# Performance work log

Measured on AMD Instinct MI355X. Metric: run time of the kernel, lower is better.

Reference implementation:

```python
import jax, jax.numpy as jnp
import numpy as np

H = 3072; NH = 24; HD = 128; MLP_D = 12288
B = 1; IMG = 1536; REF = 512; TXT = 256

def _gelu_tanh(x):
    return jax.nn.gelu(x, approximate=True)

def _ln(x, eps=1e-6):
    m = jnp.mean(x, axis=-1, keepdims=True)
    v = jnp.var(x, axis=-1, keepdims=True)
    return (x - m) * jax.lax.rsqrt(v + eps)

def _rms(x, g, eps=1e-6):
    return x * jax.lax.rsqrt(jnp.mean(x * x, axis=-1, keepdims=True) + eps) * g

def _rot_half(x):
    # interleaved rotate-half: (x0,x1,x2,x3,...) -> (-x1,x0,-x3,x2,...)
    x2 = x.reshape(x.shape[:-1] + (-1, 2))
    return jnp.stack([-x2[..., 1], x2[..., 0]], axis=-1).reshape(x.shape)

def setup_inputs():
    key = jax.random.key(0)
    ks = jax.random.split(key, 16)
    s = 0.02
    # rope tables for image tokens (interleaved layout, values repeated x2)
    inv_freq = 1.0 / (10000.0 ** (jnp.arange(0, HD // 2, dtype=jnp.float32) / (HD // 2)))
    ang = jnp.arange(IMG, dtype=jnp.float32)[:, None] * inv_freq[None, :]   # [IMG, HD//2]
    ang = jnp.repeat(ang, 2, axis=-1)                                       # [IMG, HD]
    return {
        'x':   jax.random.normal(ks[0], (B, IMG + TXT, H), jnp.float32),
        'vec': jax.random.normal(ks[1], (B, H), jnp.float32),
        'ref': jax.random.normal(ks[2], (B, REF, H), jnp.float32),
        'cos': jnp.cos(ang), 'sin': jnp.sin(ang),
        'mod_w':  jax.random.normal(ks[3], (H, 3 * H), jnp.float32) * s,
        'mod_b':  jnp.zeros((3 * H,), jnp.float32),
        'rf1_w':  jax.random.normal(ks[4], (H, H), jnp.float32) * s,
        'rf1_b':  jnp.zeros((H,), jnp.float32),
        'rf2_w':  jax.random.normal(ks[5], (H, H), jnp.float32) * s,
        'rf2_b':  jnp.zeros((H,), jnp.float32),
        'rln_g':  jnp.ones((H,), jnp.float32),
        'rln_b':  jnp.zeros((H,), jnp.float32),
        'lin1_w': jax.random.normal(ks[6], (H, 3 * H + MLP_D), jnp.float32) * s,
        'lin1_b': jnp.zeros((3 * H + MLP_D,), jnp.float32),
        'q_g':    jnp.ones((HD,), jnp.float32),
        'k_g':    jnp.ones((HD,), jnp.float32),
        'lin2_w': jax.random.normal(ks[7], (H + MLP_D, H), jnp.float32) * s,
        'lin2_b': jnp.zeros((H,), jnp.float32),
        'text_mask': jnp.ones((B, TXT), jnp.int32),
        'img_len': IMG, 'txt_len': TXT,
    }

def _forward(x, vec, ref, cos, sin, mod_w, mod_b, rf1_w, rf1_b, rf2_w, rf2_b,
             rln_g, rln_b, lin1_w, lin1_b, q_g, k_g, lin2_w, lin2_b,
             text_mask, img_len, txt_len):
    Bb = x.shape[0]
    ref_len = ref.shape[1]
    # modulation (ModulateDiT: SiLU -> Linear -> chunk(3))
    mod = jnp.dot(jax.nn.silu(vec), mod_w) + mod_b
    shift, scale, gate = jnp.split(mod, 3, axis=-1)
    x_mod = _ln(x) * (1.0 + scale[:, None]) + shift[:, None]
    # ref MLP + affine LayerNorm
    r = jnp.dot(_gelu_tanh(jnp.dot(ref, rf1_w) + rf1_b), rf2_w) + rf2_b
    r = _ln(r) * rln_g + rln_b
    # token reassembly: [img | ref | txt]
    xc = jnp.concatenate([x_mod[:, :img_len], r, x_mod[:, img_len:]], axis=1)
    h = jnp.dot(xc, lin1_w) + lin1_b
    qkv, mlp = h[..., :3 * H], h[..., 3 * H:]
    L2 = xc.shape[1]
    q, k, v = [t.reshape(Bb, L2, NH, HD) for t in jnp.split(qkv, 3, axis=-1)]
    # q drops the ref span; ref contributes K/V only
    q = jnp.concatenate([q[:, :img_len], q[:, img_len + ref_len:]], axis=1)
    q = _rms(q, q_g)
    k = _rms(k, k_g)
    # rotary only on image tokens
    c = cos[None, :, None, :]; s = sin[None, :, None, :]
    img_q = q[:, :img_len] * c + _rot_half(q[:, :img_len]) * s
    img_k = k[:, :img_len] * c + _rot_half(k[:, :img_len]) * s
    q = jnp.concatenate([img_q, q[:, img_len:]], axis=1)          # [B, Lq, NH, HD]
    k = jnp.concatenate([img_k, k[:, img_len:]], axis=1)          # [B, Lkv, NH, HD]
    # varlen mask (cu_seqlens semantics): valid attends valid, pad attends pad
    tmask = text_mask.astype(bool)
    qv  = jnp.concatenate([jnp.ones((Bb, img_len), bool), tmask], axis=1)
    kvv = jnp.concatenate([jnp.ones((Bb, img_len + ref_len), bool), tmask], axis=1)
    allowed = (qv[:, None, :, None] == kvv[:, None, None, :])     # [B,1,Lq,Lkv]
    scores = jnp.einsum('bqhd,bkhd->bhqk', q, k) * (HD ** -0.5)
    scores = jnp.where(allowed, scores, jnp.asarray(-1e9, scores.dtype))
    p = jax.nn.softmax(scores, axis=-1)
    attn = jnp.einsum('bhqk,bkhd->bqhd', p, v).reshape(Bb, img_len + txt_len, H)
    mlp = jnp.concatenate([mlp[:, :img_len], mlp[:, img_len + ref_len:]], axis=1)
    out = jnp.dot(jnp.concatenate([attn, _gelu_tanh(mlp)], axis=-1), lin2_w) + lin2_b
    return x + out * gate[:, None]

def reference(x, vec, ref, cos, sin, mod_w, mod_b, rf1_w, rf1_b, rf2_w, rf2_b,
              rln_g, rln_b, lin1_w, lin1_b, q_g, k_g, lin2_w, lin2_b,
              text_mask, img_len, txt_len):
    return _forward(x, vec, ref, cos, sin, mod_w, mod_b, rf1_w, rf1_b, rf2_w, rf2_b,
                    rln_g, rln_b, lin1_w, lin1_b, q_g, k_g, lin2_w, lin2_b,
                    text_mask, img_len, txt_len)
```

## Files before the change

kernel.cpp:

```cpp
#include <hip/hip_runtime.h>
#include <cstdint>
#include <cstddef>

typedef unsigned short u16;
typedef unsigned int   u32;
typedef __bf16 bf16_t;
typedef bf16_t bf16x8 __attribute__((ext_vector_type(8)));
typedef float  f32x4  __attribute__((ext_vector_type(4)));
typedef u16    u16x4  __attribute__((ext_vector_type(4)));


__device__ __forceinline__ float b2f(u16 b){ u32 u=((u32)b)<<16; float f; __builtin_memcpy(&f,&u,4); return f; }
__device__ __forceinline__ u16 f2b(float f){ u32 u; __builtin_memcpy(&u,&f,4); u = u + 0x7fffu + ((u>>16)&1u); return (u16)(u>>16); }
__device__ __forceinline__ float gelu_f(float x){
  float x3 = x*x*x;
  return 0.5f*x*(1.f + tanhf(0.7978845608028654f*(x + 0.044715f*x3)));
}

__device__ __forceinline__ void gload_lds16(const void* g, void* l){
  __builtin_amdgcn_global_load_lds((const __attribute__((address_space(1))) void*)g,
                                   (__attribute__((address_space(3))) void*)l, 16, 0, 0);
}

template<int NW, bool MX>
__device__ __forceinline__ float bred(float v, float* red){
  #pragma unroll
  for (int o=32;o;o>>=1){ float u=__shfl_down(v,o,64); v = MX? fmaxf(v,u) : v+u; }
  const int t = threadIdx.x;
  if ((t&63)==0) red[t>>6]=v;
  __syncthreads();
  float r = red[0];
  #pragma unroll
  for (int i=1;i<NW;i++) r = MX? fmaxf(r,red[i]) : r+red[i];
  __syncthreads();
  return r;
}

__device__ __forceinline__ void unpack8(uint4 u, float* f){
  f[0]=b2f((u16)(u.x&0xffffu)); f[1]=b2f((u16)(u.x>>16));
  f[2]=b2f((u16)(u.y&0xffffu)); f[3]=b2f((u16)(u.y>>16));
  f[4]=b2f((u16)(u.z&0xffffu)); f[5]=b2f((u16)(u.z>>16));
  f[6]=b2f((u16)(u.w&0xffffu)); f[7]=b2f((u16)(u.w>>16));
}
__device__ __forceinline__ uint4 pack8(const float* f){
  uint4 u;
  u.x = (u32)f2b(f[0]) | ((u32)f2b(f[1])<<16);
  u.y = (u32)f2b(f[2]) | ((u32)f2b(f[3])<<16);
  u.z = (u32)f2b(f[4]) | ((u32)f2b(f[5])<<16);
  u.w = (u32)f2b(f[6]) | ((u32)f2b(f[7])<<16);
  return u;
}

__global__ void modv_part(const float* __restrict__ vec, const float* __restrict__ W,
                          float* __restrict__ part){
  __shared__ float s[128];
  const int t = threadIdx.x;
  const int j = blockIdx.x*256 + t;
  const int i0 = blockIdx.y*128;
  if (t < 128){ float v = vec[i0+t]; s[t] = v/(1.f+__expf(-v)); }
  __syncthreads();
  float acc = 0.f;
  #pragma unroll 8
  for (int i=0;i<128;i++) acc += s[i]*W[(size_t)(i0+i)*9216 + j];
  part[(size_t)blockIdx.y*9216 + j] = acc;
}
__global__ void modv_reduce(const float* __restrict__ part, const float* __restrict__ mb,
                            float* __restrict__ modp){
  const int j = blockIdx.x*256 + threadIdx.x;
  float a = mb[j];
  #pragma unroll
  for (int c=0;c<24;c++) a += part[(size_t)c*9216 + j];
  modp[j] = a;
}

__global__ void convT(const float* __restrict__ W, u16* __restrict__ Wt, int Kd, int Nd){
  __shared__ float Ls[32][33];
  const int tx = threadIdx.x, ty = threadIdx.y;
  const int n0 = blockIdx.x*32, k0 = blockIdx.y*32;
  #pragma unroll
  for (int r=0;r<4;r++) Ls[ty+r*8][tx] = W[(size_t)(k0+ty+r*8)*Nd + n0+tx];
  __syncthreads();
  #pragma unroll
  for (int r=0;r<4;r++) Wt[(size_t)(n0+ty+r*8)*Kd + k0+tx] = f2b(Ls[tx][ty+r*8]);
}

__global__ void convertF2B(const float* __restrict__ src, u16* __restrict__ dst){
  const size_t i = ((size_t)blockIdx.x*256 + threadIdx.x)*4;
  const float4 v = *(const float4*)(src+i);
  u16x4 o; o.x=f2b(v.x); o.y=f2b(v.y); o.z=f2b(v.z); o.w=f2b(v.w);
  *(u16x4*)(dst+i) = o;
}

__global__ void ln_modulate(const float* __restrict__ x, const float* __restrict__ modp,
                            u16* __restrict__ xc){
  __shared__ float red[4];
  const int row = blockIdx.x, t = threadIdx.x;
  const float* xr = x + (size_t)row*3072;
  float4 v[3]; float s=0.f, ss=0.f;
  #pragma unroll
  for (int k=0;k<3;k++){
    v[k] = *(const float4*)(xr + t*4 + k*1024);
    s  += v[k].x+v[k].y+v[k].z+v[k].w;
    ss += v[k].x*v[k].x+v[k].y*v[k].y+v[k].z*v[k].z+v[k].w*v[k].w;
  }
  s  = bred<4,false>(s, red);
  ss = bred<4,false>(ss, red);
  const float mean = s*(1.f/3072.f);
  const float inv = rsqrtf(ss*(1.f/3072.f)-mean*mean + 1e-6f);
  const int orow = row<1536 ? row : row+512;
  u16* o = xc + (size_t)orow*3072;
  const float* shiftp = modp; const float* scalep = modp+3072;
  #pragma unroll
  for (int k=0;k<3;k++){
    const int j = t*4 + k*1024;
    const float4 sc = *(const float4*)(scalep+j);
    const float4 sh = *(const float4*)(shiftp+j);
    u16x4 ov;
    ov.x = f2b((v[k].x-mean)*inv*(1.f+sc.x)+sh.x);
    ov.y = f2b((v[k].y-mean)*inv*(1.f+sc.y)+sh.y);
    ov.z = f2b((v[k].z-mean)*inv*(1.f+sc.z)+sh.z);
    ov.w = f2b((v[k].w-mean)*inv*(1.f+sc.w)+sh.w);
    *(u16x4*)(o+j) = ov;
  }
}

__global__ void ln_ref(const float* __restrict__ rt, const float* __restrict__ g,
                       const float* __restrict__ b, u16* __restrict__ xc){
  __shared__ float red[4];
  const int row = blockIdx.x, t = threadIdx.x;
  const float* xr = rt + (size_t)row*3072;
  float4 v[3]; float s=0.f, ss=0.f;
  #pragma unroll
  for (int k=0;k<3;k++){
    v[k] = *(const float4*)(xr + t*4 + k*1024);
    s  += v[k].x+v[k].y+v[k].z+v[k].w;
    ss += v[k].x*v[k].x+v[k].y*v[k].y+v[k].z*v[k].z+v[k].w*v[k].w;
  }
  s  = bred<4,false>(s, red);
  ss = bred<4,false>(ss, red);
  const float mean = s*(1.f/3072.f);
  const float inv = rsqrtf(ss*(1.f/3072.f)-mean*mean + 1e-6f);
  u16* o = xc + (size_t)(1536+row)*3072;
  #pragma unroll
  for (int k=0;k<3;k++){
    const int j = t*4 + k*1024;
    const float4 gv = *(const float4*)(g+j);
    const float4 bv = *(const float4*)(b+j);
    u16x4 ov;
    ov.x = f2b((v[k].x-mean)*inv*gv.x+bv.x);
    ov.y = f2b((v[k].y-mean)*inv*gv.y+bv.y);
    ov.z = f2b((v[k].z-mean)*inv*gv.z+bv.z);
    ov.w = f2b((v[k].w-mean)*inv*gv.w+bv.w);
    *(u16x4*)(o+j) = ov;
  }
}

__global__ void qk_prep(const u16* __restrict__ h, const float* __restrict__ qg,
                        const float* __restrict__ kg, const float* __restrict__ cosb,
                        const float* __restrict__ sinb, u16* __restrict__ Q,
                        u16* __restrict__ Kb){
  __shared__ float red[4];
  const int row = blockIdx.x, hd = blockIdx.y, d = threadIdx.x;
  const u16* hr = h + (size_t)row*21504;
  const float kv = b2f(hr[3072 + hd*128 + d]);
  const bool doq = (row < 1536) || (row >= 2048);
  const float qv = doq ? b2f(hr[hd*128 + d]) : 0.f;
  float a = kv*kv, b = qv*qv;
  #pragma unroll
  for (int o=32;o;o>>=1){ a += __shfl_down(a,o,64); b += __shfl_down(b,o,64); }
  if ((d&63)==0){ red[(d>>6)*2] = a; red[(d>>6)*2+1] = b; }
  __syncthreads();
  const float kinv = rsqrtf((red[0]+red[2])*(1.f/128.f) + 1e-6f);
  const float qinv = rsqrtf((red[1]+red[3])*(1.f/128.f) + 1e-6f);
  float kn = kv*kinv*kg[d];
  float qn = qv*qinv*qg[d];
  if (row < 1536){
    const float c  = cosb[row*128 + d];
    const float sn = sinb[row*128 + d];
    const float ko = b2f(hr[3072 + hd*128 + (d^1)])*kinv*kg[d^1];
    const float qo = b2f(hr[hd*128 + (d^1)])*qinv*qg[d^1];
    const float krh = (d&1) ? ko : -ko;
    const float qrh = (d&1) ? qo : -qo;
    kn = kn*c + krh*sn;
    qn = qn*c + qrh*sn;
  }
  Kb[((size_t)hd*2304 + row)*128 + d] = f2b(kn);
  if (doq){
    const int qrow = row<1536 ? row : row-512;
    Q[((size_t)hd*1792 + qrow)*128 + d] = f2b(qn);
  }
}

__global__ void v_transpose(const u16* __restrict__ h, u16* __restrict__ VT){
  __shared__ u16 Ls[32][33];
  const int tx = threadIdx.x, ty = threadIdx.y;
  const int l0 = blockIdx.x*32, d0 = blockIdx.y*32, hd = blockIdx.z;
  #pragma unroll
  for (int r=0;r<4;r++)
    Ls[ty+r*8][tx] = h[(size_t)(l0+ty+r*8)*21504 + 6144 + hd*128 + d0 + tx];
  __syncthreads();
  #pragma unroll
  for (int r=0;r<4;r++)
    VT[((size_t)hd*128 + d0+ty+r*8)*2304 + l0 + tx] = Ls[tx][ty+r*8];
}

__global__ void gelu_mlp(const u16* __restrict__ h, u16* __restrict__ out2){
  const int q = blockIdx.x;
  const int hrow = q<1536 ? q : q+512;
  const int j = blockIdx.y*2048 + threadIdx.x*8;
  const uint4 u = *(const uint4*)(h + (size_t)hrow*21504 + 9216 + j);
  float f[8]; unpack8(u, f);
  #pragma unroll
  for (int e=0;e<8;e++) f[e] = gelu_f(f[e]);
  const uint4 o = pack8(f);
  *(uint4*)(out2 + (size_t)q*15360 + 3072 + j) = o;
}

template<int EPI>
__global__ __launch_bounds__(256)
void gemm_bt(const u16* __restrict__ A, const u16* __restrict__ Bt,
             const float* __restrict__ bias, void* __restrict__ Cv,
             int K, int ldA, int ldB, int ldC,
             long long sA, long long sB, long long sC,
             float alpha, const float* __restrict__ xres,
             const float* __restrict__ gate, const int* __restrict__ tmask)
{
  __shared__ u16 As[128*32];
  __shared__ u16 Bs[128*32];
  const int t = threadIdx.x;
  const int w = t>>6, lane = t&63;
  const int bm = blockIdx.y, bn = blockIdx.x, bz = blockIdx.z;
  const u16* Ab = A + (size_t)((long long)bz*sA) + (size_t)bm*128*ldA;
  const u16* Bb = Bt + (size_t)((long long)bz*sB) + (size_t)bn*128*ldB;
  const int wm = w>>1, wn = w&1;
  const int lr = lane&15, lk = lane>>4;
  const int row0 = t>>2, kp0 = (t&3)*8;
  char* AsB = (char*)As; char* BsB = (char*)Bs;
  const int off0 = w*1024;
  const int off1 = 4096 + w*1024;
  f32x4 acc[4][4] = {};

  for (int kt = 0; kt < K; kt += 32){
    __syncthreads();
    gload_lds16(Ab + (size_t)row0*ldA + kt + kp0,      AsB + off0);
    gload_lds16(Ab + (size_t)(row0+64)*ldA + kt + kp0, AsB + off1);
    gload_lds16(Bb + (size_t)row0*ldB + kt + kp0,      BsB + off0);
    gload_lds16(Bb + (size_t)(row0+64)*ldB + kt + kp0, BsB + off1);
    __syncthreads();
    bf16x8 av[4], bv[4];
    #pragma unroll
    for (int i=0;i<4;i++) av[i] = *(const bf16x8*)(As + (wm*64+i*16+lr)*32 + lk*8);
    #pragma unroll
    for (int j=0;j<4;j++) bv[j] = *(const bf16x8*)(Bs + (wn*64+j*16+lr)*32 + lk*8);
    #pragma unroll
    for (int i=0;i<4;i++)
      #pragma unroll
      for (int j=0;j<4;j++)
        acc[i][j] = __builtin_amdgcn_mfma_f32_16x16x32_bf16(av[i], bv[j], acc[i][j], 0,0,0);
  }

  const int mBase = bm*128 + wm*64;
  const int nBase = bn*128 + wn*64;
  #pragma unroll
  for (int i=0;i<4;i++){
    #pragma unroll
    for (int j=0;j<4;j++){
      #pragma unroll
      for (int r=0;r<4;r++){
        const int m = mBase + i*16 + lk*4 + r;
        const int n = nBase + j*16 + lr;
        const float v = acc[i][j][r];
        const long long idx = (long long)bz*sC + (long long)m*ldC + n;
        if (EPI==0){
          ((float*)Cv)[idx] = v + bias[n];
        } else if (EPI==1){
          ((u16*)Cv)[idx] = f2b(gelu_f(v + bias[n]));
        } else if (EPI==2){
          ((u16*)Cv)[idx] = f2b(v + bias[n]);
        } else {
          ((float*)Cv)[idx] = xres[(long long)m*ldC + n] + (v + bias[n])*gate[n];
        }
      }
    }
  }
}

#define G256_BAR()  __builtin_amdgcn_s_barrier()
#define G256_LGKM() do{ asm volatile("s_waitcnt lgkmcnt(0)" ::: "memory"); \
                        __builtin_amdgcn_sched_barrier(0); }while(0)

template<int CEPI>
__global__ __launch_bounds__(512,2)
void gemm256(const u16* __restrict__ A, const u16* __restrict__ Bt,
             const float* __restrict__ bias, void* __restrict__ Cv,
             int Kc, int ld, int ldC, int nbn, int ntile, long long sC, int nwg, int gm)
{
  __shared__ char smem[131072];
  const int t = threadIdx.x;
  const int wid = t>>6, lane = t&63;
  const int lr = lane&15, lk = lane>>4;
  const int wm = wid>>2, wn = wid&3;

  const int orig = blockIdx.x;
  const int q8 = nwg>>3, r8 = nwg&7;
  const int xcd = orig&7, jj = orig>>3;
  const int wg = (xcd<r8 ? xcd*(q8+1) : r8*(q8+1) + (xcd-r8)*q8) + jj;
  int sk, bm, bn;
  if (gm > 0){
    const int band = wg / (gm*nbn);
    const int rr = wg - band*(gm*nbn);
    bn = rr / gm;
    bm = band*gm + (rr - bn*gm);
    sk = 0;
  } else {
    sk = wg / ntile;
    const int rem = wg - sk*ntile;
    bm = rem / nbn; bn = rem % nbn;
  }

  const u16* Agl = A  + (size_t)bm*256*ld + (size_t)sk*Kc;
  const u16* Bgl = Bt + (size_t)bn*256*ld + (size_t)sk*Kc;
  const int NT = Kc>>6;

  const int d0 = wid*64 + lane;
  const int sr = d0>>3;
  const size_t soff = (size_t)sr*ld + (size_t)(((d0&7)^(sr&7))<<3);

  const int xsl0 = ((lk    ) ^ (lr&7))<<4;
  const int xsl1 = ((lk | 4) ^ (lr&7))<<4;

  f32x4 acc[8][4] = {};
  bf16x8 bv[4][2];

  auto STAGE = [&](const u16* g, int h, int kt, char* ldsMat){
    const u16* s0 = g + (size_t)(h*128)*ld + kt + soff;
    char* l0 = ldsMat + h*16384 + wid*1024;
    gload_lds16(s0, l0);
    gload_lds16(s0 + (size_t)64*ld, l0 + 8192);
  };

  STAGE(Agl, 0, 0, smem);
  STAGE(Agl, 1, 0, smem);
  STAGE(Bgl, 0, 0, smem + 32768);
  STAGE(Bgl, 1, 0, smem + 32768);
  if (NT > 1){
    STAGE(Bgl, 0, 64, smem + 65536 + 32768);
    STAGE(Bgl, 1, 64, smem + 65536 + 32768);
    asm volatile("s_waitcnt vmcnt(4)" ::: "memory");
  } else {
    asm volatile("s_waitcnt vmcnt(0)" ::: "memory");
  }
  G256_BAR();

#define G256_MFMA_Q(Q)                                                          \
  do{                                                                           \
    _Pragma("unroll")                                                           \
    for (int j=0;j<4;j++){                                                      \
      acc[(Q)*2+0][j] = __builtin_amdgcn_mfma_f32_16x16x32_bf16(av00, bv[j][0], acc[(Q)*2+0][j], 0,0,0); \
      acc[(Q)*2+0][j] = __builtin_amdgcn_mfma_f32_16x16x32_bf16(av01, bv[j][1], acc[(Q)*2+0][j], 0,0,0); \
      acc[(Q)*2+1][j] = __builtin_amdgcn_mfma_f32_16x16x32_bf16(av10, bv[j][0], acc[(Q)*2+1][j], 0,0,0); \
      acc[(Q)*2+1][j] = __builtin_amdgcn_mfma_f32_16x16x32_bf16(av11, bv[j][1], acc[(Q)*2+1][j], 0,0,0); \
    }                                                                           \
  }while(0)

#define G256_PHASE(Q, STG, TAILW)                                               \
  do{                                                                           \
    const char* abase = cA + (wm*128 + (Q)*32 + lr)*128;                        \
    bf16x8 av00 = *(const bf16x8*)(abase + xsl0);                               \
    bf16x8 av01 = *(const bf16x8*)(abase + xsl1);                               \
    bf16x8 av10 = *(const bf16x8*)(abase + 2048 + xsl0);                        \
    bf16x8 av11 = *(const bf16x8*)(abase + 2048 + xsl1);                        \
    if ((Q)==0){                                                                \
      _Pragma("unroll")                                                         \
      for (int j=0;j<4;j++){                                                    \
        const char* bbase = cB + (wn*64 + j*16 + lr)*128;                       \
        bv[j][0] = *(const bf16x8*)(bbase + xsl0);                              \
        bv[j][1] = *(const bf16x8*)(bbase + xsl1);                              \
      }                                                                         \
    }                                                                           \
    STG;                                                                        \
    G256_BAR();                                                                 \
    G256_LGKM();                                                                \
    __builtin_amdgcn_s_setprio(1);                                              \
    G256_MFMA_Q(Q);                                                             \
    __builtin_amdgcn_s_setprio(0);                                              \
    TAILW;                                                                      \
    G256_BAR();                                                                 \
  }while(0)

  for (int tt = 0; tt < NT; ++tt){
    char* cA = smem + (tt&1)*65536;
    char* cB = cA + 32768;
    char* nA = smem + ((tt+1)&1)*65536;
    const int kt1 = (tt+1)<<6, kt2 = (tt+2)<<6;
    const bool stA = (tt+1) < NT, stB = (tt+2) < NT;

    G256_PHASE(0, if (stA) STAGE(Agl, 0, kt1, nA), );
    G256_PHASE(1, if (stA) STAGE(Agl, 1, kt1, nA), );
    G256_PHASE(2, if (stB) STAGE(Bgl, 0, kt2, cB), );
    G256_PHASE(3, if (stB) STAGE(Bgl, 1, kt2, cB),
               if (stB)      { asm volatile("s_waitcnt vmcnt(4)" ::: "memory"); }
               else if (stA) { asm volatile("s_waitcnt vmcnt(0)" ::: "memory"); } );
  }
#undef G256_PHASE
#undef G256_MFMA_Q

  const int mB = bm*256 + wm*128 + lk*4;
  const int nB = bn*256 + wn*64 + lr;
  #pragma unroll
  for (int fi=0; fi<8; fi++){
    #pragma unroll
    for (int j=0; j<4; j++){
      const int n = nB + j*16;
      const float bb = (CEPI==0) ? bias[n] : 0.f;
      #pragma unroll
      for (int r=0;r<4;r++){
        const int m = mB + fi*16 + r;
        if (CEPI==0){
          ((u16*)Cv)[(size_t)m*ldC + n] = f2b(acc[fi][j][r] + bb);
        } else {
          ((float*)Cv)[(size_t)sk*sC + (size_t)m*ldC + n] = acc[fi][j][r];
        }
      }
    }
  }
}

__global__ __launch_bounds__(512)
void flash_attn(const u16* __restrict__ Qb, const u16* __restrict__ Kb,
                const u16* __restrict__ VT, const int* __restrict__ tmask,
                u16* __restrict__ out2)
{
  __shared__ __attribute__((aligned(16))) char smf[114688];
  char* Qs  = smf;
  char* Ks0 = smf + 32768;
  char* Vs0 = smf + 65536;
  char* Ps  = smf + 98304;
  const int t = threadIdx.x, wid = t>>6, lane = t&63;
  const int lr = lane&15, hi = lane>>4;
  const int head = blockIdx.y, qt = blockIdx.x;
  const int q0 = qt*128;
  const u16* Qg = Qb + ((size_t)head*1792 + q0)*128;
  const u16* Kg = Kb + (size_t)head*2304*128;
  const u16* Vg = VT + (size_t)head*128*2304;
  const float SCALE = 0.08838834764831845f;

  u32 kbits = 0;
  #pragma unroll
  for (int i=0;i<16;i++) kbits |= (u32)(tmask[i*16 + lr] != 0) << i;
  int fqr[4];
  #pragma unroll
  for (int r=0;r<4;r++){
    const int q = q0 + wid*16 + hi*4 + r;
    fqr[r] = (q < 1536) ? 1 : (tmask[q-1536] != 0);
  }

  #pragma unroll
  for (int c=0;c<4;c++){
    const int s = c*512 + wid*64 + lane;
    const int row = s>>4, dsl = s&15;
    gload_lds16(Qg + (size_t)row*128 + ((dsl ^ (row&7))<<3),
                Qs + (size_t)(c*512 + wid*64)*16);
  }
  #pragma unroll
  for (int c=0;c<2;c++){
    const int s = c*512 + wid*64 + lane;
    { const int row = s>>4, dsl = s&15;
      gload_lds16(Kg + (size_t)row*128 + ((dsl ^ (row&7))<<3),
                  Ks0 + (size_t)(c*512 + wid*64)*16); }
    { const int row = s>>3, dsl = s&7;
      gload_lds16(Vg + (size_t)row*2304 + ((dsl ^ (row&7))<<3),
                  Vs0 + (size_t)(c*512 + wid*64)*16); }
  }
  asm volatile("s_waitcnt vmcnt(0)" ::: "memory");
  __syncthreads();

  bf16x8 av[4];
  {
    const int row = wid*16 + lr;
    #pragma unroll
    for (int ks=0;ks<4;ks++)
      av[ks] = *(const bf16x8*)(Qs + row*256 + (((ks*4+hi) ^ (row&7))<<4));
  }

  f32x4 acc[8] = {};
  float m_[4], l_[4];
  #pragma unroll
  for (int r=0;r<4;r++){ m_[r] = -3e38f; l_[r] = 0.f; }

  for (int kt = 0; kt < 36; ++kt){
    char* Kc = Ks0 + (kt&1)*16384;
    char* Vc = Vs0 + (kt&1)*16384;
    if (kt+1 < 36){
      char* Kn = Ks0 + ((kt+1)&1)*16384;
      char* Vn = Vs0 + ((kt+1)&1)*16384;
      #pragma unroll
      for (int c=0;c<2;c++){
        const int s = c*512 + wid*64 + lane;
        { const int row = s>>4, dsl = s&15;
          gload_lds16(Kg + (size_t)((kt+1)*64 + row)*128 + ((dsl ^ (row&7))<<3),
                      Kn + (size_t)(c*512 + wid*64)*16); }
        { const int row = s>>3, dsl = s&7;
          gload_lds16(Vg + (size_t)row*2304 + (kt+1)*64 + ((dsl ^ (row&7))<<3),
                      Vn + (size_t)(c*512 + wid*64)*16); }
      }
    }
    f32x4 sacc[4] = {};
    #pragma unroll
    for (int ks=0;ks<4;ks++){
      #pragma unroll
      for (int j=0;j<4;j++){
        const int row = j*16 + lr;
        bf16x8 bk = *(const bf16x8*)(Kc + row*256 + (((ks*4+hi) ^ (row&7))<<4));
        sacc[j] = __builtin_amdgcn_mfma_f32_16x16x32_bf16(av[ks], bk, sacc[j], 0,0,0);
      }
    }
    int gkj[4];
    #pragma unroll
    for (int j=0;j<4;j++)
      gkj[j] = (kt < 32) ? 1 : (int)((kbits >> ((kt-32)*4 + j)) & 1u);
    float p[4][4]; bool alw[4][4];
    float mt[4] = {-3e38f,-3e38f,-3e38f,-3e38f};
    #pragma unroll
    for (int j=0;j<4;j++){
      #pragma unroll
      for (int r=0;r<4;r++){
        const float s = sacc[j][r]*SCALE;
        const bool a = (fqr[r] == gkj[j]);
        alw[j][r] = a; p[j][r] = s;
        if (a) mt[r] = fmaxf(mt[r], s);
      }
    }
    #pragma unroll
    for (int r=0;r<4;r++){
      #pragma unroll
      for (int o=1;o<16;o<<=1) mt[r] = fmaxf(mt[r], __shfl_xor(mt[r], o, 64));
      const float nm = fmaxf(m_[r], mt[r]);
      const float cr = __expf(m_[r] - nm);
      m_[r] = nm;
      l_[r] *= cr;
      #pragma unroll
      for (int jp=0;jp<8;jp++) acc[jp][r] *= cr;
    }
    float rs[4] = {0.f,0.f,0.f,0.f};
    #pragma unroll
    for (int j=0;j<4;j++){
      #pragma unroll
      for (int r=0;r<4;r++){
        const float pv = alw[j][r] ? __expf(p[j][r] - m_[r]) : 0.f;
        p[j][r] = pv; rs[r] += pv;
      }
    }
    #pragma unroll
    for (int r=0;r<4;r++){
      #pragma unroll
      for (int o=1;o<16;o<<=1) rs[r] += __shfl_xor(rs[r], o, 64);
      l_[r] += rs[r];
    }
    #pragma unroll
    for (int j=0;j<4;j++){
      #pragma unroll
      for (int r=0;r<4;r++){
        const int q = wid*16 + hi*4 + r;
        const int k = j*16 + lr;
        *(u16*)(Ps + q*128 + (((k>>3) ^ (q&7))<<4) + (k&7)*2) = f2b(p[j][r]);
      }
    }
    asm volatile("s_waitcnt lgkmcnt(0)" ::: "memory");
    __builtin_amdgcn_sched_barrier(0);
    bf16x8 pa[2];
    {
      const int row = wid*16 + lr;
      #pragma unroll
      for (int ks2=0;ks2<2;ks2++)
        pa[ks2] = *(const bf16x8*)(Ps + row*128 + (((ks2*4+hi) ^ (row&7))<<4));
    }
    #pragma unroll
    for (int ks2=0;ks2<2;ks2++){
      #pragma unroll
      for (int jp=0;jp<8;jp++){
        const int row = jp*16 + lr;
        bf16x8 bvv = *(const bf16x8*)(Vc + row*128 + (((ks2*4+hi) ^ (row&7))<<4));
        acc[jp] = __builtin_amdgcn_mfma_f32_16x16x32_bf16(pa[ks2], bvv, acc[jp], 0,0,0);
      }
    }
    asm volatile("s_waitcnt vmcnt(0)" ::: "memory");
    __syncthreads();
  }

  float inv[4];
  #pragma unroll
  for (int r=0;r<4;r++) inv[r] = 1.f/l_[r];
  #pragma unroll
  for (int jp=0;jp<8;jp++){
    #pragma unroll
    for (int r=0;r<4;r++){
      const size_t q = q0 + wid*16 + hi*4 + r;
      out2[q*15360 + head*128 + jp*16 + lr] = f2b(acc[jp][r]*inv[r]);
    }
  }
}

__global__ void lin2_fin(const float* __restrict__ P, const float* __restrict__ x,
                         const float* __restrict__ bias, const float* __restrict__ gate,
                         float* __restrict__ out){
  const size_t e = ((size_t)blockIdx.x*256 + threadIdx.x)*4;
  const int n = (int)(e % 3072);
  const size_t S = (size_t)1792*3072;
  const float4 p0 = *(const float4*)(P + e);
  const float4 p1 = *(const float4*)(P + S + e);
  const float4 p2 = *(const float4*)(P + 2*S + e);
  const float4 bb = *(const float4*)(bias + n);
  const float4 gg = *(const float4*)(gate + n);
  const float4 xv = *(const float4*)(x + e);
  float4 o;
  o.x = xv.x + (p0.x+p1.x+p2.x+bb.x)*gg.x;
  o.y = xv.y + (p0.y+p1.y+p2.y+bb.y)*gg.y;
  o.z = xv.z + (p0.z+p1.z+p2.z+bb.z)*gg.z;
  o.w = xv.w + (p0.w+p1.w+p2.w+bb.w)*gg.w;
  *(float4*)(out + e) = o;
}

extern "C" void kernel_launch(void* const* d_in, const int* in_sizes, int n_in,
                              void* d_out, int out_size, void* d_ws, size_t ws_size,
                              hipStream_t stream)
{
  (void)in_sizes; (void)n_in; (void)out_size; (void)ws_size;
  const float* x     = (const float*)d_in[0];
  const float* vec   = (const float*)d_in[1];
  const float* ref   = (const float*)d_in[2];
  const float* cosb  = (const float*)d_in[3];
  const float* sinb  = (const float*)d_in[4];
  const float* mod_w = (const float*)d_in[5];
  const float* mod_b = (const float*)d_in[6];
  const float* rf1_w = (const float*)d_in[7];
  const float* rf1_b = (const float*)d_in[8];
  const float* rf2_w = (const float*)d_in[9];
  const float* rf2_b = (const float*)d_in[10];
  const float* rln_g = (const float*)d_in[11];
  const float* rln_b = (const float*)d_in[12];
  const float* lin1_w= (const float*)d_in[13];
  const float* lin1_b= (const float*)d_in[14];
  const float* q_g   = (const float*)d_in[15];
  const float* k_g   = (const float*)d_in[16];
  const float* lin2_w= (const float*)d_in[17];
  const float* lin2_b= (const float*)d_in[18];
  const int*   tmask = (const int*)d_in[19];
  float* out = (float*)d_out;
  char* ws = (char*)d_ws;

  float* modp = (float*)(ws + 0);
  float* part = (float*)(ws + 36864);
  u16*  w2t   = (u16*)(ws + 921600);
  u16*  Qb    = (u16*)(ws + 95293440ll);
  u16*  Kb    = (u16*)(ws + 106303488ll);
  u16*  VT    = (u16*)(ws + 120459264ll);
  u16*  out2  = (u16*)(ws + 134615040ll);
  u16*  w1t   = (u16*)(ws + 189665280ll);
  u16*  xc    = (u16*)(ws + 321785856ll);
  u16*  rf1t  = (u16*)(ws + 335941632ll);
  u16*  rf2t  = (u16*)(ws + 354816000ll);
  u16*  refb  = (u16*)(ws + 373690368ll);
  u16*  tb    = (u16*)(ws + 376836096ll);
  float* rtmp = (float*)(ws + 379981824ll);
  u16*  hbuf  = (u16*)(ws + 335941632ll);
  float* p2b  = (float*)(ws + 189665280ll);

  modv_part<<<dim3(36,24),256,0,stream>>>(vec, mod_w, part);
  modv_reduce<<<36,256,0,stream>>>(part, mod_b, modp);
  convT<<<dim3(96,96), dim3(32,8),0,stream>>>(rf1_w, rf1t, 3072, 3072);
  convT<<<dim3(96,96), dim3(32,8),0,stream>>>(rf2_w, rf2t, 3072, 3072);
  convT<<<dim3(672,96),dim3(32,8),0,stream>>>(lin1_w, w1t, 3072, 21504);
  convT<<<dim3(96,480),dim3(32,8),0,stream>>>(lin2_w, w2t, 15360, 3072);
  convertF2B<<<1536,256,0,stream>>>(ref, refb);
  ln_modulate<<<1792,256,0,stream>>>(x, modp, xc);
  gemm_bt<1><<<dim3(24,4,1),256,0,stream>>>(refb, rf1t, rf1_b, tb, 3072,3072,3072,3072,
                                            0,0,0, 0.f, nullptr,nullptr,nullptr);
  gemm_bt<0><<<dim3(24,4,1),256,0,stream>>>(tb, rf2t, rf2_b, rtmp, 3072,3072,3072,3072,
                                            0,0,0, 0.f, nullptr,nullptr,nullptr);
  ln_ref<<<512,256,0,stream>>>(rtmp, rln_g, rln_b, xc);
  gemm256<0><<<756,512,0,stream>>>(xc, w1t, lin1_b, hbuf, 3072, 3072, 21504, 84, 756, 0, 756, 3);
  qk_prep<<<dim3(2304,24),128,0,stream>>>(hbuf, q_g, k_g, cosb, sinb, Qb, Kb);
  v_transpose<<<dim3(72,4,24),dim3(32,8),0,stream>>>(hbuf, VT);
  gelu_mlp<<<dim3(1792,6),256,0,stream>>>(hbuf, out2);
  flash_attn<<<dim3(14,24),512,0,stream>>>(Qb, Kb, VT, tmask, out2);
  gemm256<1><<<252,512,0,stream>>>(out2, w2t, nullptr, p2b, 5120, 15360, 3072, 12, 84,
                                   (long long)1792*3072, 252, 0);
  lin2_fin<<<5376,256,0,stream>>>(p2b, x, lin2_b, modp + 6144, out);
}
```

Baseline: 1.011 ms.

## Split-K the ref-path GEMMs, fuse GELU into lin1 epilogue, drop LDS wait

The two small ref-path GEMMs (512x3072x3072) now run split-K over 6 slices, which raises the block count from 96 to 576, and separate kernels sum the partials and apply bias plus GELU or bias. The lin1 GEMM epilogue now applies GELU to the MLP columns and writes them straight into the lin2 input buffer, so the separate gelu_mlp pass and its re-read of the hidden buffer go away. The explicit lgkmcnt wait after the barrier in the big GEMM phase is also removed, and the barrier becomes an inline-asm s_barrier. The split-K path adds traffic for the fp32 partials, and dropping the LDS wait risks reading LDS before the loads complete.

```diff
diff --git a/kernel.cpp b/kernel.cpp
--- a/kernel.cpp
+++ b/kernel.cpp
@@ -41,14 +41,6 @@
   f[2]=b2f((u16)(u.y&0xffffu)); f[3]=b2f((u16)(u.y>>16));
   f[4]=b2f((u16)(u.z&0xffffu)); f[5]=b2f((u16)(u.z>>16));
   f[6]=b2f((u16)(u.w&0xffffu)); f[7]=b2f((u16)(u.w>>16));
-}
-__device__ __forceinline__ uint4 pack8(const float* f){
-  uint4 u;
-  u.x = (u32)f2b(f[0]) | ((u32)f2b(f[1])<<16);
-  u.y = (u32)f2b(f[2]) | ((u32)f2b(f[3])<<16);
-  u.z = (u32)f2b(f[4]) | ((u32)f2b(f[5])<<16);
-  u.w = (u32)f2b(f[6]) | ((u32)f2b(f[7])<<16);
-  return u;
 }
 
 __global__ void modv_part(const float* __restrict__ vec, const float* __restrict__ W,
@@ -204,26 +196,12 @@
     VT[((size_t)hd*128 + d0+ty+r*8)*2304 + l0 + tx] = Ls[tx][ty+r*8];
 }
 
-__global__ void gelu_mlp(const u16* __restrict__ h, u16* __restrict__ out2){
-  const int q = blockIdx.x;
-  const int hrow = q<1536 ? q : q+512;
-  const int j = blockIdx.y*2048 + threadIdx.x*8;
-  const uint4 u = *(const uint4*)(h + (size_t)hrow*21504 + 9216 + j);
-  float f[8]; unpack8(u, f);
-  #pragma unroll
-  for (int e=0;e<8;e++) f[e] = gelu_f(f[e]);
-  const uint4 o = pack8(f);
-  *(uint4*)(out2 + (size_t)q*15360 + 3072 + j) = o;
-}
-
 template<int EPI>
 __global__ __launch_bounds__(256)
 void gemm_bt(const u16* __restrict__ A, const u16* __restrict__ Bt,
              const float* __restrict__ bias, void* __restrict__ Cv,
              int K, int ldA, int ldB, int ldC,
-             long long sA, long long sB, long long sC,
-             float alpha, const float* __restrict__ xres,
-             const float* __restrict__ gate, const int* __restrict__ tmask)
+             long long sA, long long sB, long long sC)
 {
   __shared__ u16 As[128*32];
   __shared__ u16 Bs[128*32];
@@ -271,28 +249,55 @@
         const int n = nBase + j*16 + lr;
         const float v = acc[i][j][r];
         const long long idx = (long long)bz*sC + (long long)m*ldC + n;
-        if (EPI==0){
-          ((float*)Cv)[idx] = v + bias[n];
-        } else if (EPI==1){
-          ((u16*)Cv)[idx] = f2b(gelu_f(v + bias[n]));
-        } else if (EPI==2){
+        if (EPI==6){
+          ((float*)Cv)[idx] = v;
+        } else {
           ((u16*)Cv)[idx] = f2b(v + bias[n]);
-        } else {
-          ((float*)Cv)[idx] = xres[(long long)m*ldC + n] + (v + bias[n])*gate[n];
         }
       }
     }
   }
 }
 
-#define G256_BAR()  __builtin_amdgcn_s_barrier()
-#define G256_LGKM() do{ asm volatile("s_waitcnt lgkmcnt(0)" ::: "memory"); \
-                        __builtin_amdgcn_sched_barrier(0); }while(0)
+__global__ void comb_gelu(const float* __restrict__ P, const float* __restrict__ b,
+                          u16* __restrict__ o){
+  const size_t e = ((size_t)blockIdx.x*256 + threadIdx.x)*4;
+  const int n = (int)(e % 3072);
+  const size_t S = (size_t)512*3072;
+  float4 a = *(const float4*)(P + e);
+  #pragma unroll
+  for (int c=1;c<6;c++){
+    const float4 p = *(const float4*)(P + c*S + e);
+    a.x+=p.x; a.y+=p.y; a.z+=p.z; a.w+=p.w;
+  }
+  const float4 bb = *(const float4*)(b + n);
+  u16x4 ov;
+  ov.x = f2b(gelu_f(a.x+bb.x)); ov.y = f2b(gelu_f(a.y+bb.y));
+  ov.z = f2b(gelu_f(a.z+bb.z)); ov.w = f2b(gelu_f(a.w+bb.w));
+  *(u16x4*)(o + e) = ov;
+}
+__global__ void comb_bias(const float* __restrict__ P, const float* __restrict__ b,
+                          float* __restrict__ o){
+  const size_t e = ((size_t)blockIdx.x*256 + threadIdx.x)*4;
+  const int n = (int)(e % 3072);
+  const size_t S = (size_t)512*3072;
+  float4 a = *(const float4*)(P + e);
+  #pragma unroll
+  for (int c=1;c<6;c++){
+    const float4 p = *(const float4*)(P + c*S + e);
+    a.x+=p.x; a.y+=p.y; a.z+=p.z; a.w+=p.w;
+  }
+  const float4 bb = *(const float4*)(b + n);
+  float4 ov; ov.x=a.x+bb.x; ov.y=a.y+bb.y; ov.z=a.z+bb.z; ov.w=a.w+bb.w;
+  *(float4*)(o + e) = ov;
+}
+
+#define G256_BAR()  asm volatile("s_barrier" ::: "memory")
 
 template<int CEPI>
 __global__ __launch_bounds__(512,2)
 void gemm256(const u16* __restrict__ A, const u16* __restrict__ Bt,
-             const float* __restrict__ bias, void* __restrict__ Cv,
+             const float* __restrict__ bias, void* __restrict__ Cv, void* __restrict__ Cv2,
              int Kc, int ld, int ldC, int nbn, int ntile, long long sC, int nwg, int gm)
 {
   __shared__ char smem[131072];
@@ -380,7 +385,6 @@
     }                                                                           \
     STG;                                                                        \
     G256_BAR();                                                                 \
-    G256_LGKM();                                                                \
     __builtin_amdgcn_s_setprio(1);                                              \
     G256_MFMA_Q(Q);                                                             \
     __builtin_amdgcn_s_setprio(0);                                              \
@@ -412,14 +416,20 @@
     #pragma unroll
     for (int j=0; j<4; j++){
       const int n = nB + j*16;
-      const float bb = (CEPI==0) ? bias[n] : 0.f;
+      const float bb = (CEPI==2) ? bias[n] : 0.f;
       #pragma unroll
       for (int r=0;r<4;r++){
         const int m = mB + fi*16 + r;
-        if (CEPI==0){
-          ((u16*)Cv)[(size_t)m*ldC + n] = f2b(acc[fi][j][r] + bb);
+        if (CEPI==1){
+          ((float*)Cv)[(size_t)sk*sC + (size_t)m*ldC + n] = acc[fi][j][r];
         } else {
-          ((float*)Cv)[(size_t)sk*sC + (size_t)m*ldC + n] = acc[fi][j][r];
+          if (n < 9216){
+            ((u16*)Cv)[(size_t)m*ldC + n] = f2b(acc[fi][j][r] + bb);
+          } else {
+            const int qm = (m < 1536) ? m : (m >= 2048 ? m - 512 : -1);
+            if (qm >= 0)
+              ((u16*)Cv2)[(size_t)qm*15360 + 3072 + (n - 9216)] = f2b(gelu_f(acc[fi][j][r] + bb));
+          }
         }
       }
     }
@@ -663,6 +673,7 @@
   u16*  refb  = (u16*)(ws + 373690368ll);
   u16*  tb    = (u16*)(ws + 376836096ll);
   float* rtmp = (float*)(ws + 379981824ll);
+  float* rp   = (float*)(ws + 386273280ll);
   u16*  hbuf  = (u16*)(ws + 335941632ll);
   float* p2b  = (float*)(ws + 189665280ll);
 
@@ -674,17 +685,18 @@
   convT<<<dim3(96,480),dim3(32,8),0,stream>>>(lin2_w, w2t, 15360, 3072);
   convertF2B<<<1536,256,0,stream>>>(ref, refb);
   ln_modulate<<<1792,256,0,stream>>>(x, modp, xc);
-  gemm_bt<1><<<dim3(24,4,1),256,0,stream>>>(refb, rf1t, rf1_b, tb, 3072,3072,3072,3072,
-                                            0,0,0, 0.f, nullptr,nullptr,nullptr);
-  gemm_bt<0><<<dim3(24,4,1),256,0,stream>>>(tb, rf2t, rf2_b, rtmp, 3072,3072,3072,3072,
-                                            0,0,0, 0.f, nullptr,nullptr,nullptr);
+  gemm_bt<6><<<dim3(24,4,6),256,0,stream>>>(refb, rf1t, nullptr, rp, 512, 3072,3072,3072,
+                                            512,512, (long long)512*3072);
+  comb_gelu<<<1536,256,0,stream>>>(rp, rf1_b, tb);
+  gemm_bt<6><<<dim3(24,4,6),256,0,stream>>>(tb, rf2t, nullptr, rp, 512, 3072,3072,3072,
+                                            512,512, (long long)512*3072);
+  comb_bias<<<1536,256,0,stream>>>(rp, rf2_b, rtmp);
   ln_ref<<<512,256,0,stream>>>(rtmp, rln_g, rln_b, xc);
-  gemm256<0><<<756,512,0,stream>>>(xc, w1t, lin1_b, hbuf, 3072, 3072, 21504, 84, 756, 0, 756, 3);
+  gemm256<2><<<756,512,0,stream>>>(xc, w1t, lin1_b, hbuf, out2, 3072, 3072, 21504, 84, 756, 0, 756, 3);
   qk_prep<<<dim3(2304,24),128,0,stream>>>(hbuf, q_g, k_g, cosb, sinb, Qb, Kb);
   v_transpose<<<dim3(72,4,24),dim3(32,8),0,stream>>>(hbuf, VT);
-  gelu_mlp<<<dim3(1792,6),256,0,stream>>>(hbuf, out2);
   flash_attn<<<dim3(14,24),512,0,stream>>>(Qb, Kb, VT, tmask, out2);
-  gemm256<1><<<252,512,0,stream>>>(out2, w2t, nullptr, p2b, 5120, 15360, 3072, 12, 84,
+  gemm256<1><<<252,512,0,stream>>>(out2, w2t, nullptr, p2b, nullptr, 5120, 15360, 3072, 12, 84,
                                    (long long)1792*3072, 252, 0);
   lin2_fin<<<5376,256,0,stream>>>(p2b, x, lin2_b, modp + 6144, out);
 }
```

Measured after the change: 964.4 us. 1.05x faster.
